# Kernel tuning notes

Hardware: AMD Instinct MI355X
Metric: run time of the kernel (lower is better)

Reference implementation:

```python
import jax, jax.numpy as jnp
import numpy as np

N, D, H, E, TOP_K = 4096, 1024, 4096, 8, 2


def setup_inputs() -> dict:
    key = jax.random.key(0)
    ks = jax.random.split(key, 5)
    s_in = 1.0 / np.sqrt(D)
    s_hid = 1.0 / np.sqrt(H)
    return {
        "x": jax.random.normal(ks[0], (N, D), jnp.float32),
        "Wg": jax.random.normal(ks[1], (D, E), jnp.float32) * s_in,
        "bg": jnp.zeros((E,), jnp.float32),
        "W1": jax.random.normal(ks[2], (E, D, H), jnp.float32) * s_in,
        "b1": jnp.zeros((E, H), jnp.float32),
        "W2": jax.random.normal(ks[3], (E, H, D), jnp.float32) * s_hid,
        "b2": jnp.zeros((E, D), jnp.float32),
    }


def reference(x, Wg, bg, W1, b1, W2, b2):
    # Gating: softmax over experts, then top-k selection (weights NOT renormalized,
    # matching the original which multiplies raw topk softmax values).
    gate_scores = jax.nn.softmax(x @ Wg + bg, axis=-1)            # [N, E]
    topk_vals, topk_idx = jax.lax.top_k(gate_scores, TOP_K)       # [N, k]

    # Dense per-token combine weights: w[n, e] = sum of topk_vals where topk_idx == e
    n_ar = jnp.arange(x.shape[0])[:, None]
    w = jnp.zeros_like(gate_scores).at[n_ar, topk_idx].add(topk_vals)  # [N, E]

    # Expert FFN for every expert (dense grouped-GEMM form), weighted combine.
    h = jax.nn.relu(jnp.einsum('nd,edh->neh', x, W1) + b1)        # [N, E, H]
    y = jnp.einsum('neh,ehd->ned', h, W2) + b2                    # [N, E, D]
    return jnp.einsum('ne,ned->nd', w, y)                         # [N, D]
```

## Files before the change

kernel.cpp:

```cpp
#include <hip/hip_runtime.h>
#include <hip/hip_bf16.h>
#include <stdint.h>

#define NT 4096
#define DD 1024
#define HH 4096
#define NEXP 8

typedef __attribute__((ext_vector_type(8))) short bf16x8;
typedef __attribute__((ext_vector_type(4))) float f32x4;

#define GLOAD16(g, l) __builtin_amdgcn_global_load_lds( \
    (const __attribute__((address_space(1))) void*)(g), \
    (__attribute__((address_space(3))) void*)(l), 16, 0, 0)

__device__ inline ushort f2b(float f) {
  union { float f; uint32_t u; } v; v.f = f;
  uint32_t u = v.u;
  return (ushort)((u + 0x7fffu + ((u >> 16) & 1u)) >> 16);
}

__global__ __launch_bounds__(256) void gating_kernel(
    const float* __restrict__ x, const float* __restrict__ Wg,
    const float* __restrict__ bg, float* __restrict__ wgt,
    int* __restrict__ tidx, float* __restrict__ tval, int* __restrict__ counts) {
  int gw = (blockIdx.x * 256 + threadIdx.x) >> 6;
  int lane = threadIdx.x & 63;
  if (gw >= NT) return;
  const float* xr = x + (size_t)gw * DD;
  float acc[NEXP];
#pragma unroll
  for (int e = 0; e < NEXP; e++) acc[e] = 0.f;
  for (int d = lane; d < DD; d += 64) {
    float xv = xr[d];
    const float* wr = Wg + (size_t)d * NEXP;
#pragma unroll
    for (int e = 0; e < NEXP; e++) acc[e] += xv * wr[e];
  }
#pragma unroll
  for (int off = 32; off > 0; off >>= 1) {
#pragma unroll
    for (int e = 0; e < NEXP; e++) acc[e] += __shfl_xor(acc[e], off, 64);
  }
  float l[NEXP], m = -1e30f;
#pragma unroll
  for (int e = 0; e < NEXP; e++) { l[e] = acc[e] + bg[e]; m = fmaxf(m, l[e]); }
  float s = 0.f;
#pragma unroll
  for (int e = 0; e < NEXP; e++) { l[e] = expf(l[e] - m); s += l[e]; }
  float inv = 1.f / s;
  float v1 = -1.f, v2 = -1.f; int i1 = -1, i2 = -1;
#pragma unroll
  for (int e = 0; e < NEXP; e++) {
    float p = l[e] * inv;
    if (p > v1) { v2 = v1; i2 = i1; v1 = p; i1 = e; }
    else if (p > v2) { v2 = p; i2 = e; }
  }
  if (lane < NEXP) {
    float w = (lane == i1) ? v1 : ((lane == i2) ? v2 : 0.f);
    wgt[(size_t)gw * NEXP + lane] = w;
  }
  if (lane == 0) {
    tidx[gw * 2 + 0] = i1; tval[gw * 2 + 0] = v1;
    tidx[gw * 2 + 1] = i2; tval[gw * 2 + 1] = v2;
    atomicAdd(&counts[i1], 1);
    atomicAdd(&counts[i2], 1);
  }
}

__global__ void scan_kernel(const int* __restrict__ counts, int* __restrict__ base) {
  int b = 0;
#pragma unroll
  for (int e = 0; e < NEXP; e++) { base[e] = b; b += ((counts[e] + 127) >> 7) << 7; }
}

__global__ __launch_bounds__(256) void scatter_kernel(
    const int* __restrict__ tidx, const float* __restrict__ tval,
    const int* __restrict__ base, int* __restrict__ cursor,
    int* __restrict__ perm, float* __restrict__ pairw) {
  int t = blockIdx.x * 256 + threadIdx.x;
  if (t >= NT) return;
#pragma unroll
  for (int k = 0; k < 2; k++) {
    int e = tidx[t * 2 + k];
    int pos = atomicAdd(&cursor[e], 1);
    int p = base[e] + pos;
    perm[p] = t;
    pairw[p] = tval[t * 2 + k];
  }
}

__global__ __launch_bounds__(256) void cvt_x_kernel(
    const float* __restrict__ in, ushort* __restrict__ out, int n) {
  int i = (blockIdx.x * 256 + threadIdx.x) * 4;
  if (i >= n) return;
  float4 v = *(const float4*)(in + i);
  ushort4 o; o.x = f2b(v.x); o.y = f2b(v.y); o.z = f2b(v.z); o.w = f2b(v.w);
  *(ushort4*)(out + i) = o;
}

__global__ __launch_bounds__(256) void transpose_cvt64_kernel(
    const float* __restrict__ in, ushort* __restrict__ out, int R, int C) {
  __shared__ __align__(16) ushort T[64 * 68];
  size_t eo = (size_t)blockIdx.z * (size_t)R * C;
  in += eo; out += eo;
  int r0 = blockIdx.y * 64, c0 = blockIdx.x * 64;
  int t = threadIdx.x;
  int lr = t >> 4;
  int lc = (t & 15) * 4;
#pragma unroll
  for (int i = 0; i < 4; i++) {
    int r = lr + i * 16;
    float4 v = *(const float4*)(in + (size_t)(r0 + r) * C + c0 + lc);
    ushort4 o; o.x = f2b(v.x); o.y = f2b(v.y); o.z = f2b(v.z); o.w = f2b(v.w);
    int cs = lc ^ (((r >> 3) & 7) << 3);
    *(ushort4*)&T[r * 68 + cs] = o;
  }
  __syncthreads();
#pragma unroll
  for (int it = 0; it < 2; it++) {
    int task = it * 256 + t;
    int c = task >> 3;
    int rr0 = (task & 7) * 8;
    uint w[4];
#pragma unroll
    for (int j = 0; j < 4; j++) {
      int ra = rr0 + 2 * j, rb = ra + 1;
      uint a = T[ra * 68 + (c ^ (((ra >> 3) & 7) << 3))];
      uint b = T[rb * 68 + (c ^ (((rb >> 3) & 7) << 3))];
      w[j] = a | (b << 16);
    }
    *(uint4*)(out + (size_t)(c0 + c) * R + r0 + rr0) = make_uint4(w[0], w[1], w[2], w[3]);
  }
}

template <int MODE, bool SPARSE, int SPLITS>
__global__ __launch_bounds__(256) void gemm_bt_kernel(
    const ushort* __restrict__ A, const ushort* __restrict__ BtAll,
    const float* __restrict__ biasAll, void* __restrict__ Cout,
    const int* __restrict__ perm, const float* __restrict__ pairw,
    const float* __restrict__ wgtDense,
    const int* __restrict__ base, const int* __restrict__ cnt,
    int Nn, int K, int eFixed) {
  const int BK = 32;
  __shared__ __align__(16) ushort As[128 * BK];
  __shared__ __align__(16) ushort Bs[128 * BK];
  int e, sp, m0;
  if (SPARSE) {
    e = blockIdx.z / SPLITS;
    sp = blockIdx.z % SPLITS;
    if ((int)blockIdx.y * 128 >= cnt[e]) return;
    m0 = base[e] + blockIdx.y * 128;
  } else {
    e = eFixed; sp = 0;
    m0 = blockIdx.y * 128;
  }
  int n0 = blockIdx.x * 128;
  const ushort* Bt = SPARSE ? BtAll + (size_t)e * Nn * K : BtAll;
  const float* bias = biasAll + (size_t)e * Nn;

  int tid = threadIdx.x, wv = tid >> 6, lane = tid & 63;
  int sr = lane >> 2;
  int sc = (lane & 3) * 8;
  int ar0 = m0 + wv * 32 + sr, ar1 = ar0 + 16;
  int64_t gr0, gr1;
  if (SPARSE && MODE == 1) { gr0 = perm[ar0]; gr1 = perm[ar1]; }
  else { gr0 = ar0; gr1 = ar1; }
  const ushort* gA0 = A + gr0 * (int64_t)K + sc;
  const ushort* gA1 = A + gr1 * (int64_t)K + sc;
  const ushort* gB0 = Bt + (int64_t)(n0 + wv * 32 + sr) * K + sc;
  const ushort* gB1 = gB0 + (int64_t)16 * K;
  ushort* lA0 = &As[(wv * 32) * BK];
  ushort* lA1 = &As[(wv * 32 + 16) * BK];
  ushort* lB0 = &Bs[(wv * 32) * BK];
  ushort* lB1 = &Bs[(wv * 32 + 16) * BK];

  int wr = (wv >> 1) * 64;
  int wc = (wv & 1) * 64;
  int lr = lane & 15;
  int kq = (lane >> 4) * 8;

  f32x4 acc[4][4];
#pragma unroll
  for (int i = 0; i < 4; i++)
#pragma unroll
    for (int j = 0; j < 4; j++) acc[i][j] = (f32x4)(0.f);

  int kb = (K / SPLITS) * sp, ke = kb + K / SPLITS;
  for (int k0 = kb; k0 < ke; k0 += BK) {
    __syncthreads();
    GLOAD16(gA0 + k0, lA0);
    GLOAD16(gA1 + k0, lA1);
    GLOAD16(gB0 + k0, lB0);
    GLOAD16(gB1 + k0, lB1);
    __syncthreads();
    bf16x8 af[4], bfr[4];
#pragma unroll
    for (int i = 0; i < 4; i++)
      af[i] = *(const bf16x8*)&As[(wr + i * 16 + lr) * BK + kq];
#pragma unroll
    for (int j = 0; j < 4; j++)
      bfr[j] = *(const bf16x8*)&Bs[(wc + j * 16 + lr) * BK + kq];
#pragma unroll
    for (int i = 0; i < 4; i++)
#pragma unroll
      for (int j = 0; j < 4; j++)
        acc[i][j] = __builtin_amdgcn_mfma_f32_16x16x32_bf16(af[i], bfr[j],
                                                            acc[i][j], 0, 0, 0);
  }

  int rq = (lane >> 4) * 4;
  if (MODE == 1) {
    ushort* Cb = (ushort*)Cout;
#pragma unroll
    for (int i = 0; i < 4; i++) {
#pragma unroll
      for (int r = 0; r < 4; r++) {
        int row = m0 + wr + i * 16 + rq + r;
#pragma unroll
        for (int j = 0; j < 4; j++) {
          int col = n0 + wc + j * 16 + lr;
          float v = acc[i][j][r] + bias[col];
          Cb[(size_t)row * Nn + col] = f2b(fmaxf(v, 0.f));
        }
      }
    }
  } else {
    float* Co = (float*)Cout;
#pragma unroll
    for (int i = 0; i < 4; i++) {
#pragma unroll
      for (int r = 0; r < 4; r++) {
        int row = m0 + wr + i * 16 + rq + r;
        if (SPARSE) {
          float w = pairw[row];
          if (w != 0.f) {
            int t = perm[row];
#pragma unroll
            for (int j = 0; j < 4; j++) {
              int col = n0 + wc + j * 16 + lr;
              float bterm = (sp == 0) ? bias[col] : 0.f;
              atomicAdd(&Co[(size_t)t * DD + col], w * (acc[i][j][r] + bterm));
            }
          }
        } else {
          float w = wgtDense[(size_t)row * NEXP + e];
          if (w != 0.f) {
#pragma unroll
            for (int j = 0; j < 4; j++) {
              int col = n0 + wc + j * 16 + lr;
              Co[(size_t)row * Nn + col] += w * (acc[i][j][r] + bias[col]);
            }
          }
        }
      }
    }
  }
}

extern "C" void kernel_launch(void* const* d_in, const int* in_sizes, int n_in,
                              void* d_out, int out_size, void* d_ws,
                              size_t ws_size, hipStream_t stream) {
  const float* x  = (const float*)d_in[0];
  const float* Wg = (const float*)d_in[1];
  const float* bg = (const float*)d_in[2];
  const float* W1 = (const float*)d_in[3];
  const float* b1 = (const float*)d_in[4];
  const float* W2 = (const float*)d_in[5];
  const float* b2 = (const float*)d_in[6];
  float* out = (float*)d_out;
  char* ws = (char*)d_ws;

  hipMemsetAsync(d_out, 0, (size_t)out_size * sizeof(float), stream);

  const size_t XB_SZ   = (size_t)NT * DD * 2;
  const size_t WT_SZ   = (size_t)NEXP * DD * HH * 2;
  const size_t HB_ROWS = 9216;
  const size_t HB_SZ   = HB_ROWS * HH * 2;
  const size_t W1T_OFF = XB_SZ;
  const size_t W2T_OFF = W1T_OFF + WT_SZ;
  const size_t HB_OFF  = W2T_OFF + WT_SZ;
  const size_t SM_OFF  = HB_OFF + HB_SZ;
  const size_t TIER_A_NEED = SM_OFF + 275456;

  if (ws_size >= TIER_A_NEED) {
    ushort* xb   = (ushort*)ws;
    ushort* w1t  = (ushort*)(ws + W1T_OFF);
    ushort* w2t  = (ushort*)(ws + W2T_OFF);
    ushort* hbuf = (ushort*)(ws + HB_OFF);
    char* sm = ws + SM_OFF;
    int*   counts = (int*)(sm + 0);
    int*   cursor = (int*)(sm + 128);
    int*   base   = (int*)(sm + 256);
    int*   tidx   = (int*)(sm + 1024);
    float* tval   = (float*)(sm + 1024 + 32768);
    int*   perm   = (int*)(sm + 68608);
    float* pairw  = (float*)(sm + 105472);
    float* wgt    = (float*)(sm + 143360);

    hipMemsetAsync(sm, 0, 142336, stream);

    gating_kernel<<<NT / 4, 256, 0, stream>>>(x, Wg, bg, wgt, tidx, tval, counts);
    cvt_x_kernel<<<(NT * DD / 4 + 255) / 256, 256, 0, stream>>>(x, xb, NT * DD);
    scan_kernel<<<1, 1, 0, stream>>>(counts, base);
    scatter_kernel<<<NT / 256, 256, 0, stream>>>(tidx, tval, base, cursor, perm, pairw);

    transpose_cvt64_kernel<<<dim3(HH / 64, DD / 64, NEXP), 256, 0, stream>>>(W1, w1t, DD, HH);
    transpose_cvt64_kernel<<<dim3(DD / 64, HH / 64, NEXP), 256, 0, stream>>>(W2, w2t, HH, DD);

    gemm_bt_kernel<1, true, 1><<<dim3(HH / 128, NT / 128, NEXP), 256, 0, stream>>>(
        xb, w1t, b1, hbuf, perm, pairw, nullptr, base, counts, HH, DD, 0);
    gemm_bt_kernel<2, true, 4><<<dim3(DD / 128, NT / 128, NEXP * 4), 256, 0, stream>>>(
        hbuf, w2t, b2, out, perm, pairw, nullptr, base, counts, DD, HH, 0);
    return;
  }

  ushort* xb  = (ushort*)ws;
  ushort* hb  = (ushort*)(ws + (8u << 20));
  ushort* w1t = (ushort*)(ws + (42u << 20));
  ushort* w2t = (ushort*)(ws + (51u << 20));
  char* sm2 = ws + (59u << 20);
  int*   tidx   = (int*)(sm2);
  float* tval   = (float*)(sm2 + 32768);
  int*   counts = (int*)(sm2 + 65536);
  float* wgt    = (float*)(ws + (60u << 20));

  gating_kernel<<<NT / 4, 256, 0, stream>>>(x, Wg, bg, wgt, tidx, tval, counts);
  cvt_x_kernel<<<(NT * DD / 4 + 255) / 256, 256, 0, stream>>>(x, xb, NT * DD);

  for (int e = 0; e < NEXP; e++) {
    transpose_cvt64_kernel<<<dim3(HH / 64, DD / 64, 1), 256, 0, stream>>>(
        W1 + (size_t)e * DD * HH, w1t, DD, HH);
    gemm_bt_kernel<1, false, 1><<<dim3(HH / 128, NT / 128, 1), 256, 0, stream>>>(
        xb, w1t, b1, hb, nullptr, nullptr, nullptr, nullptr, nullptr, HH, DD, e);
    transpose_cvt64_kernel<<<dim3(DD / 64, HH / 64, 1), 256, 0, stream>>>(
        W2 + (size_t)e * HH * DD, w2t, HH, DD);
    gemm_bt_kernel<2, false, 1><<<dim3(DD / 128, NT / 128, 1), 256, 0, stream>>>(
        hb, w2t, b2, out, nullptr, nullptr, wgt, nullptr, nullptr, DD, HH, e);
  }
}
```

Measured before the change: 865.3 us.

## Double-buffer GEMM LDS with swizzle, replace split-K atomics with combine kernel

The GEMM kernel gets double-buffered LDS tiles, so the next K-slice is prefetched while MFMAs run on the current one, and an XOR swizzle on the LDS column index to cut bank conflicts. The second GEMM drops its 4-way split-K and atomicAdd scatter. Instead it writes weighted per-pair rows into a ybuf that reuses the W1-transposed workspace, and a new combine kernel sums each token's two rows using positions recorded by the scatter kernel. This removes the output memset and the float atomics, but the second GEMM now launches a quarter as many blocks and an extra buffer pass is added.

Measured after the change: 738.2 us. -14.7%, faster.

```diff
diff --git a/kernel.cpp b/kernel.cpp
--- a/kernel.cpp
+++ b/kernel.cpp
@@ -77,7 +77,8 @@
 __global__ __launch_bounds__(256) void scatter_kernel(
     const int* __restrict__ tidx, const float* __restrict__ tval,
     const int* __restrict__ base, int* __restrict__ cursor,
-    int* __restrict__ perm, float* __restrict__ pairw) {
+    int* __restrict__ perm, float* __restrict__ pairw,
+    int* __restrict__ pos0, int* __restrict__ pos1) {
   int t = blockIdx.x * 256 + threadIdx.x;
   if (t >= NT) return;
 #pragma unroll
@@ -87,6 +88,7 @@
     int p = base[e] + pos;
     perm[p] = t;
     pairw[p] = tval[t * 2 + k];
+    if (k == 0) pos0[t] = p; else pos1[t] = p;
   }
 }
 
@@ -134,7 +136,7 @@
   }
 }
 
-template <int MODE, bool SPARSE, int SPLITS>
+template <int MODE, bool SPARSE>
 __global__ __launch_bounds__(256) void gemm_bt_kernel(
     const ushort* __restrict__ A, const ushort* __restrict__ BtAll,
     const float* __restrict__ biasAll, void* __restrict__ Cout,
@@ -143,16 +145,15 @@
     const int* __restrict__ base, const int* __restrict__ cnt,
     int Nn, int K, int eFixed) {
   const int BK = 32;
-  __shared__ __align__(16) ushort As[128 * BK];
-  __shared__ __align__(16) ushort Bs[128 * BK];
-  int e, sp, m0;
+  __shared__ __align__(16) ushort As[2][128 * BK];
+  __shared__ __align__(16) ushort Bs[2][128 * BK];
+  int e, m0;
   if (SPARSE) {
-    e = blockIdx.z / SPLITS;
-    sp = blockIdx.z % SPLITS;
+    e = blockIdx.z;
     if ((int)blockIdx.y * 128 >= cnt[e]) return;
     m0 = base[e] + blockIdx.y * 128;
   } else {
-    e = eFixed; sp = 0;
+    e = eFixed;
     m0 = blockIdx.y * 128;
   }
   int n0 = blockIdx.x * 128;
@@ -161,24 +162,23 @@
 
   int tid = threadIdx.x, wv = tid >> 6, lane = tid & 63;
   int sr = lane >> 2;
-  int sc = (lane & 3) * 8;
+  int csw = ((lane & 3) ^ ((sr >> 1) & 3)) * 8;
   int ar0 = m0 + wv * 32 + sr, ar1 = ar0 + 16;
   int64_t gr0, gr1;
   if (SPARSE && MODE == 1) { gr0 = perm[ar0]; gr1 = perm[ar1]; }
   else { gr0 = ar0; gr1 = ar1; }
-  const ushort* gA0 = A + gr0 * (int64_t)K + sc;
-  const ushort* gA1 = A + gr1 * (int64_t)K + sc;
-  const ushort* gB0 = Bt + (int64_t)(n0 + wv * 32 + sr) * K + sc;
+  const ushort* gA0 = A + gr0 * (int64_t)K + csw;
+  const ushort* gA1 = A + gr1 * (int64_t)K + csw;
+  const ushort* gB0 = Bt + (int64_t)(n0 + wv * 32 + sr) * K + csw;
   const ushort* gB1 = gB0 + (int64_t)16 * K;
-  ushort* lA0 = &As[(wv * 32) * BK];
-  ushort* lA1 = &As[(wv * 32 + 16) * BK];
-  ushort* lB0 = &Bs[(wv * 32) * BK];
-  ushort* lB1 = &Bs[(wv * 32 + 16) * BK];
+  int lds0 = (wv * 32) * BK;
+  int lds1 = lds0 + 16 * BK;
 
   int wr = (wv >> 1) * 64;
   int wc = (wv & 1) * 64;
   int lr = lane & 15;
   int kq = (lane >> 4) * 8;
+  int kqp = kq ^ (((lr >> 1) & 3) << 3);
 
   f32x4 acc[4][4];
 #pragma unroll
@@ -186,27 +186,36 @@
 #pragma unroll
     for (int j = 0; j < 4; j++) acc[i][j] = (f32x4)(0.f);
 
-  int kb = (K / SPLITS) * sp, ke = kb + K / SPLITS;
-  for (int k0 = kb; k0 < ke; k0 += BK) {
+  GLOAD16(gA0, &As[0][lds0]);
+  GLOAD16(gA1, &As[0][lds1]);
+  GLOAD16(gB0, &Bs[0][lds0]);
+  GLOAD16(gB1, &Bs[0][lds1]);
+
+  const int nIter = K / BK;
+  int buf = 0;
+  for (int it = 0; it < nIter; ++it) {
     __syncthreads();
-    GLOAD16(gA0 + k0, lA0);
-    GLOAD16(gA1 + k0, lA1);
-    GLOAD16(gB0 + k0, lB0);
-    GLOAD16(gB1 + k0, lB1);
-    __syncthreads();
+    if (it + 1 < nIter) {
+      int ko = (it + 1) * BK;
+      GLOAD16(gA0 + ko, &As[buf ^ 1][lds0]);
+      GLOAD16(gA1 + ko, &As[buf ^ 1][lds1]);
+      GLOAD16(gB0 + ko, &Bs[buf ^ 1][lds0]);
+      GLOAD16(gB1 + ko, &Bs[buf ^ 1][lds1]);
+    }
     bf16x8 af[4], bfr[4];
 #pragma unroll
     for (int i = 0; i < 4; i++)
-      af[i] = *(const bf16x8*)&As[(wr + i * 16 + lr) * BK + kq];
+      af[i] = *(const bf16x8*)&As[buf][(wr + i * 16 + lr) * BK + kqp];
 #pragma unroll
     for (int j = 0; j < 4; j++)
-      bfr[j] = *(const bf16x8*)&Bs[(wc + j * 16 + lr) * BK + kq];
+      bfr[j] = *(const bf16x8*)&Bs[buf][(wc + j * 16 + lr) * BK + kqp];
 #pragma unroll
     for (int i = 0; i < 4; i++)
 #pragma unroll
       for (int j = 0; j < 4; j++)
         acc[i][j] = __builtin_amdgcn_mfma_f32_16x16x32_bf16(af[i], bfr[j],
                                                             acc[i][j], 0, 0, 0);
+    buf ^= 1;
   }
 
   int rq = (lane >> 4) * 4;
@@ -234,14 +243,10 @@
         int row = m0 + wr + i * 16 + rq + r;
         if (SPARSE) {
           float w = pairw[row];
-          if (w != 0.f) {
-            int t = perm[row];
-#pragma unroll
-            for (int j = 0; j < 4; j++) {
-              int col = n0 + wc + j * 16 + lr;
-              float bterm = (sp == 0) ? bias[col] : 0.f;
-              atomicAdd(&Co[(size_t)t * DD + col], w * (acc[i][j][r] + bterm));
-            }
+#pragma unroll
+          for (int j = 0; j < 4; j++) {
+            int col = n0 + wc + j * 16 + lr;
+            Co[(size_t)row * Nn + col] = w * (acc[i][j][r] + bias[col]);
           }
         } else {
           float w = wgtDense[(size_t)row * NEXP + e];
@@ -256,6 +261,17 @@
       }
     }
   }
+}
+
+__global__ __launch_bounds__(256) void combine_kernel(
+    const float* __restrict__ ybuf, const int* __restrict__ pos0,
+    const int* __restrict__ pos1, float* __restrict__ out) {
+  int t = blockIdx.x;
+  int d = threadIdx.x * 4;
+  const float4 a = *(const float4*)(ybuf + (size_t)pos0[t] * DD + d);
+  const float4 b = *(const float4*)(ybuf + (size_t)pos1[t] * DD + d);
+  float4 o; o.x = a.x + b.x; o.y = a.y + b.y; o.z = a.z + b.z; o.w = a.w + b.w;
+  *(float4*)(out + (size_t)t * DD + d) = o;
 }
 
 extern "C" void kernel_launch(void* const* d_in, const int* in_sizes, int n_in,
@@ -271,8 +287,6 @@
   float* out = (float*)d_out;
   char* ws = (char*)d_ws;
 
-  hipMemsetAsync(d_out, 0, (size_t)out_size * sizeof(float), stream);
-
   const size_t XB_SZ   = (size_t)NT * DD * 2;
   const size_t WT_SZ   = (size_t)NEXP * DD * HH * 2;
   const size_t HB_ROWS = 9216;
@@ -288,6 +302,7 @@
     ushort* w1t  = (ushort*)(ws + W1T_OFF);
     ushort* w2t  = (ushort*)(ws + W2T_OFF);
     ushort* hbuf = (ushort*)(ws + HB_OFF);
+    float*  ybuf = (float*)(ws + W1T_OFF);
     char* sm = ws + SM_OFF;
     int*   counts = (int*)(sm + 0);
     int*   cursor = (int*)(sm + 128);
@@ -297,21 +312,25 @@
     int*   perm   = (int*)(sm + 68608);
     float* pairw  = (float*)(sm + 105472);
     float* wgt    = (float*)(sm + 143360);
+    int*   pos0   = (int*)(sm + 180224);
+    int*   pos1   = (int*)(sm + 196608);
 
     hipMemsetAsync(sm, 0, 142336, stream);
 
     gating_kernel<<<NT / 4, 256, 0, stream>>>(x, Wg, bg, wgt, tidx, tval, counts);
     cvt_x_kernel<<<(NT * DD / 4 + 255) / 256, 256, 0, stream>>>(x, xb, NT * DD);
     scan_kernel<<<1, 1, 0, stream>>>(counts, base);
-    scatter_kernel<<<NT / 256, 256, 0, stream>>>(tidx, tval, base, cursor, perm, pairw);
+    scatter_kernel<<<NT / 256, 256, 0, stream>>>(tidx, tval, base, cursor,
+                                                 perm, pairw, pos0, pos1);
 
     transpose_cvt64_kernel<<<dim3(HH / 64, DD / 64, NEXP), 256, 0, stream>>>(W1, w1t, DD, HH);
     transpose_cvt64_kernel<<<dim3(DD / 64, HH / 64, NEXP), 256, 0, stream>>>(W2, w2t, HH, DD);
 
-    gemm_bt_kernel<1, true, 1><<<dim3(HH / 128, NT / 128, NEXP), 256, 0, stream>>>(
+    gemm_bt_kernel<1, true><<<dim3(HH / 128, NT / 128, NEXP), 256, 0, stream>>>(
         xb, w1t, b1, hbuf, perm, pairw, nullptr, base, counts, HH, DD, 0);
-    gemm_bt_kernel<2, true, 4><<<dim3(DD / 128, NT / 128, NEXP * 4), 256, 0, stream>>>(
-        hbuf, w2t, b2, out, perm, pairw, nullptr, base, counts, DD, HH, 0);
+    gemm_bt_kernel<2, true><<<dim3(DD / 128, NT / 128, NEXP), 256, 0, stream>>>(
+        hbuf, w2t, b2, ybuf, nullptr, pairw, nullptr, base, counts, DD, HH, 0);
+    combine_kernel<<<NT, 256, 0, stream>>>(ybuf, pos0, pos1, out);
     return;
   }
 
@@ -323,19 +342,22 @@
   int*   tidx   = (int*)(sm2);
   float* tval   = (float*)(sm2 + 32768);
   int*   counts = (int*)(sm2 + 65536);
+  int*   pos0   = (int*)(sm2 + 131072);
+  int*   pos1   = (int*)(sm2 + 163840);
   float* wgt    = (float*)(ws + (60u << 20));
 
+  hipMemsetAsync(d_out, 0, (size_t)out_size * sizeof(float), stream);
   gating_kernel<<<NT / 4, 256, 0, stream>>>(x, Wg, bg, wgt, tidx, tval, counts);
   cvt_x_kernel<<<(NT * DD / 4 + 255) / 256, 256, 0, stream>>>(x, xb, NT * DD);
 
   for (int e = 0; e < NEXP; e++) {
     transpose_cvt64_kernel<<<dim3(HH / 64, DD / 64, 1), 256, 0, stream>>>(
         W1 + (size_t)e * DD * HH, w1t, DD, HH);
-    gemm_bt_kernel<1, false, 1><<<dim3(HH / 128, NT / 128, 1), 256, 0, stream>>>(
+    gemm_bt_kernel<1, false><<<dim3(HH / 128, NT / 128, 1), 256, 0, stream>>>(
         xb, w1t, b1, hb, nullptr, nullptr, nullptr, nullptr, nullptr, HH, DD, e);
     transpose_cvt64_kernel<<<dim3(DD / 64, HH / 64, 1), 256, 0, stream>>>(
         W2 + (size_t)e * HH * DD, w2t, HH, DD);
-    gemm_bt_kernel<2, false, 1><<<dim3(DD / 128, NT / 128, 1), 256, 0, stream>>>(
+    gemm_bt_kernel<2, false><<<dim3(DD / 128, NT / 128, 1), 256, 0, stream>>>(
         hb, w2t, b2, out, nullptr, nullptr, wgt, nullptr, nullptr, DD, HH, e);
   }
 }
```
